# Performance work log

Hardware: AMD Instinct MI355X
Metric: run time of the kernel (lower is better)

Reference implementation:

```python
import jax, jax.numpy as jnp
import numpy as np

N = 50000        # num_nodes
E = 1_600_000    # num_edges (before self loops)
IN = 128         # in_channels
C = 16           # out_channels per head
H = 4            # heads
ED = 16          # edge_dim
SLOPE = 0.2      # LeakyReLU negative slope


def setup_inputs() -> dict:
    key = jax.random.key(0)
    ks = jax.random.split(key, 9)
    x = jax.random.normal(ks[0], (N, IN), jnp.float32)
    edge_index = jax.random.randint(ks[1], (2, E), 0, N)
    edge_attr = jax.random.normal(ks[2], (E, ED), jnp.float32)
    # GATConv parameters (PyG layout): node lin (no bias), attention vectors, edge lin
    W = jax.random.normal(ks[3], (IN, H * C), jnp.float32) / np.float32(np.sqrt(IN))
    att_src = jax.random.normal(ks[4], (H, C), jnp.float32) / np.float32(np.sqrt(C))
    att_dst = jax.random.normal(ks[5], (H, C), jnp.float32) / np.float32(np.sqrt(C))
    W_edge = jax.random.normal(ks[6], (ED, H * C), jnp.float32) / np.float32(np.sqrt(ED))
    att_edge = jax.random.normal(ks[7], (H, C), jnp.float32) / np.float32(np.sqrt(C))
    bias = jnp.zeros((H * C,), jnp.float32)
    return {"x": x, "edge_index": edge_index, "edge_attr": edge_attr,
            "W": W, "att_src": att_src, "att_dst": att_dst,
            "W_edge": W_edge, "att_edge": att_edge, "bias": bias}


def reference(x, edge_index, edge_attr, W, att_src, att_dst, W_edge, att_edge, bias):
    num_nodes = x.shape[0]
    # GATLayer: add self loops (PyG fills self-loop edge_attr with 1.0)
    loops = jnp.arange(num_nodes, dtype=edge_index.dtype)
    ei = jnp.concatenate([edge_index, jnp.stack([loops, loops])], axis=1)
    ea = jnp.concatenate(
        [edge_attr, jnp.ones((num_nodes, edge_attr.shape[1]), edge_attr.dtype)], axis=0)
    src, dst = ei[0], ei[1]  # messages flow src -> dst
    # eval mode: feat_dropout / edge_dropout are no-ops
    h = (x @ W).reshape(num_nodes, H, C)              # [N,H,C]
    a_src = jnp.einsum('nhc,hc->nh', h, att_src)       # [N,H]
    a_dst = jnp.einsum('nhc,hc->nh', h, att_dst)       # [N,H]
    e = (ea @ W_edge).reshape(-1, H, C)                # [E',H,C]
    a_e = jnp.einsum('ehc,hc->eh', e, att_edge)        # [E',H]
    alpha = a_src[src] + a_dst[dst] + a_e              # per-edge logits [E',H]
    alpha = jax.nn.leaky_relu(alpha, SLOPE)
    # segment softmax over incoming edges of each dst node (every node has a self loop)
    amax = jax.ops.segment_max(alpha, dst, num_segments=num_nodes)
    ex = jnp.exp(alpha - amax[dst])
    denom = jax.ops.segment_sum(ex, dst, num_segments=num_nodes)
    att = ex / denom[dst]                              # [E',H]
    # scatter-add aggregation of weighted source features
    out = jax.ops.segment_sum(att[:, :, None] * h[src], dst, num_segments=num_nodes)
    return out.reshape(num_nodes, H * C) + bias        # concat heads + bias
```

## Files before the change

kernel.cpp:

```cpp
#include <hip/hip_runtime.h>
#include <hip/hip_bf16.h>
#include <cstdint>

#define IN_CH 128
#define HC    64
#define ED    16
#define SLOPE 0.2f

__device__ __forceinline__ uint32_t f2bf(float x) {
  uint32_t b = __float_as_uint(x);
  return (b + 0x7fffu + ((b >> 16) & 1u)) >> 16;
}
__device__ __forceinline__ float bf2f(uint32_t h) {
  return __uint_as_float(h << 16);
}

__global__ __launch_bounds__(256) void k_node(
    const float* __restrict__ x, const float* __restrict__ W,
    const float* __restrict__ att_src_p, const float* __restrict__ att_dst_p,
    float* __restrict__ h, float* __restrict__ a_src, float* __restrict__ a_dst,
    int N)
{
  int lane = threadIdx.x & 63;
  int gw = (blockIdx.x * blockDim.x + threadIdx.x) >> 6;
  int nwaves = (gridDim.x * blockDim.x) >> 6;
  float asv = att_src_p[lane];
  float adv = att_dst_p[lane];
  for (int n0 = gw * 4; n0 < N; n0 += nwaves * 4) {
    int n1 = min(n0 + 1, N - 1), n2 = min(n0 + 2, N - 1), n3 = min(n0 + 3, N - 1);
    const float4* xa = (const float4*)(x + (size_t)n0 * IN_CH);
    const float4* xb = (const float4*)(x + (size_t)n1 * IN_CH);
    const float4* xc = (const float4*)(x + (size_t)n2 * IN_CH);
    const float4* xd = (const float4*)(x + (size_t)n3 * IN_CH);
    float acc0 = 0.f, acc1 = 0.f, acc2 = 0.f, acc3 = 0.f;
#pragma unroll 4
    for (int k4 = 0; k4 < IN_CH / 4; k4++) {
      float4 va = xa[k4], vb = xb[k4], vc = xc[k4], vd = xd[k4];
      float w0 = W[(k4 * 4 + 0) * HC + lane];
      float w1 = W[(k4 * 4 + 1) * HC + lane];
      float w2 = W[(k4 * 4 + 2) * HC + lane];
      float w3 = W[(k4 * 4 + 3) * HC + lane];
      acc0 += va.x * w0 + va.y * w1 + va.z * w2 + va.w * w3;
      acc1 += vb.x * w0 + vb.y * w1 + vb.z * w2 + vb.w * w3;
      acc2 += vc.x * w0 + vc.y * w1 + vc.z * w2 + vc.w * w3;
      acc3 += vd.x * w0 + vd.y * w1 + vd.z * w2 + vd.w * w3;
    }
    h[(size_t)n0 * HC + lane] = acc0;
    if (n0 + 1 < N) h[(size_t)n1 * HC + lane] = acc1;
    if (n0 + 2 < N) h[(size_t)n2 * HC + lane] = acc2;
    if (n0 + 3 < N) h[(size_t)n3 * HC + lane] = acc3;
    float s0 = acc0 * asv, s1 = acc1 * asv, s2 = acc2 * asv, s3 = acc3 * asv;
    float d0 = acc0 * adv, d1 = acc1 * adv, d2 = acc2 * adv, d3 = acc3 * adv;
#pragma unroll
    for (int m = 1; m < 16; m <<= 1) {
      s0 += __shfl_xor(s0, m); s1 += __shfl_xor(s1, m);
      s2 += __shfl_xor(s2, m); s3 += __shfl_xor(s3, m);
      d0 += __shfl_xor(d0, m); d1 += __shfl_xor(d1, m);
      d2 += __shfl_xor(d2, m); d3 += __shfl_xor(d3, m);
    }
    if ((lane & 15) == 0) {
      int hh = lane >> 4;
      a_src[(size_t)n0 * 4 + hh] = s0; a_dst[(size_t)n0 * 4 + hh] = d0;
      if (n0 + 1 < N) { a_src[(size_t)n1 * 4 + hh] = s1; a_dst[(size_t)n1 * 4 + hh] = d1; }
      if (n0 + 2 < N) { a_src[(size_t)n2 * 4 + hh] = s2; a_dst[(size_t)n2 * 4 + hh] = d2; }
      if (n0 + 3 < N) { a_src[(size_t)n3 * 4 + hh] = s3; a_dst[(size_t)n3 * 4 + hh] = d3; }
    }
  }
}

__global__ __launch_bounds__(256) void k_hist(const int* __restrict__ dst, int E,
                                              int* __restrict__ deg)
{
  int e = blockIdx.x * 256 + threadIdx.x;
  if (e < E) atomicAdd(&deg[dst[e]], 1);
}

__global__ __launch_bounds__(256) void k_scan_a(const int* __restrict__ deg, int N,
                                                int* __restrict__ rowptr,
                                                int* __restrict__ blksums)
{
  __shared__ int tsum[256];
  int tid = threadIdx.x;
  int base = blockIdx.x * 2048 + tid * 8;
  int pre[8];
  int s = 0;
#pragma unroll
  for (int j = 0; j < 8; j++) {
    int idx = base + j;
    int v = (idx < N) ? deg[idx] : 0;
    pre[j] = s; s += v;
  }
  tsum[tid] = s;
  __syncthreads();
  for (int offm = 1; offm < 256; offm <<= 1) {
    int t = (tid >= offm) ? tsum[tid - offm] : 0;
    __syncthreads();
    tsum[tid] += t;
    __syncthreads();
  }
  int excl = tsum[tid] - s;
#pragma unroll
  for (int j = 0; j < 8; j++) {
    int idx = base + j;
    if (idx < N) rowptr[idx] = excl + pre[j];
  }
  if (tid == 255) blksums[blockIdx.x] = tsum[255];
}

__global__ void k_scan_b(int* __restrict__ blksums, int NB)
{
  if (threadIdx.x == 0 && blockIdx.x == 0) {
    int run = 0;
    for (int b = 0; b < NB; b++) { int t = blksums[b]; blksums[b] = run; run += t; }
  }
}

__global__ __launch_bounds__(256) void k_scan_c(int* __restrict__ rowptr,
                                                const int* __restrict__ blksums,
                                                int N, int E)
{
  int i = blockIdx.x * 256 + threadIdx.x;
  if (i < N) rowptr[i] += blksums[i >> 11];
  if (i == 0) rowptr[N] = E;
}

__global__ __launch_bounds__(256) void k_edge3(
    const int* __restrict__ ei, const float* __restrict__ ea,
    const float* __restrict__ W_edge, const float* __restrict__ att_edge,
    const float* __restrict__ a_src, const float* __restrict__ a_dst,
    const int* __restrict__ rowptr, int* __restrict__ cursor,
    uint4* __restrict__ pay, int E)
{
  __shared__ float ve[ED * 4];
  if (threadIdx.x < 64) {
    int d = threadIdx.x >> 2, hh = threadIdx.x & 3;
    float s = 0.f;
#pragma unroll
    for (int c = 0; c < 16; c++) s += W_edge[d * HC + hh * 16 + c] * att_edge[hh * 16 + c];
    ve[d * 4 + hh] = s;
  }
  __syncthreads();
  int e = blockIdx.x * 256 + threadIdx.x;
  if (e >= E) return;
  int sn = ei[e], dn = ei[E + e];
  float4 as4 = *(const float4*)(a_src + (size_t)sn * 4);
  float4 ad4 = *(const float4*)(a_dst + (size_t)dn * 4);
  const float4* ea4 = (const float4*)(ea + (size_t)e * ED);
  float4 q0 = ea4[0], q1 = ea4[1], q2 = ea4[2], q3 = ea4[3];
  float eav[16] = {q0.x,q0.y,q0.z,q0.w, q1.x,q1.y,q1.z,q1.w,
                   q2.x,q2.y,q2.z,q2.w, q3.x,q3.y,q3.z,q3.w};
  float ae0 = 0.f, ae1 = 0.f, ae2 = 0.f, ae3 = 0.f;
#pragma unroll
  for (int d = 0; d < ED; d++) {
    float v = eav[d];
    ae0 += v * ve[d * 4 + 0]; ae1 += v * ve[d * 4 + 1];
    ae2 += v * ve[d * 4 + 2]; ae3 += v * ve[d * 4 + 3];
  }
  float al0 = as4.x + ad4.x + ae0;
  float al1 = as4.y + ad4.y + ae1;
  float al2 = as4.z + ad4.z + ae2;
  float al3 = as4.w + ad4.w + ae3;
  al0 = al0 > 0.f ? al0 : SLOPE * al0;
  al1 = al1 > 0.f ? al1 : SLOPE * al1;
  al2 = al2 > 0.f ? al2 : SLOPE * al2;
  al3 = al3 > 0.f ? al3 : SLOPE * al3;
  int pos = rowptr[dn] + atomicAdd(&cursor[dn], 1);
  uint4 r;
  r.x = (uint32_t)sn;
  r.y = f2bf(__expf(al0)) | (f2bf(__expf(al1)) << 16);
  r.z = f2bf(__expf(al2)) | (f2bf(__expf(al3)) << 16);
  r.w = 0u;
  pay[pos] = r;
}

__global__ __launch_bounds__(256) void k_agg3(
    const float* __restrict__ h,
    const float* __restrict__ a_src, const float* __restrict__ a_dst,
    const float* __restrict__ W_edge, const float* __restrict__ att_edge,
    const float* __restrict__ bias, const int* __restrict__ rowptr,
    const uint4* __restrict__ pay, float* __restrict__ out, int N)
{
  __shared__ float aes[4];
  if (threadIdx.x < 4) {
    int hh = threadIdx.x;
    float s = 0.f;
    for (int d = 0; d < ED; d++) {
      float vd = 0.f;
#pragma unroll
      for (int c = 0; c < 16; c++) vd += W_edge[d * HC + hh * 16 + c] * att_edge[hh * 16 + c];
      s += vd;
    }
    aes[hh] = s;
  }
  __syncthreads();
  int lane = threadIdx.x & 63;
  int n = blockIdx.x * 4 + (threadIdx.x >> 6);
  if (n >= N) return;
  int hq = lane >> 4;
  int b = rowptr[n], e = rowptr[n + 1];
  float acc = 0.f, den = 0.f;
  int p = b;
  for (; p + 3 < e; p += 4) {
    uint4 r0 = pay[p], r1 = pay[p + 1], r2 = pay[p + 2], r3 = pay[p + 3];
    uint32_t w0 = (hq & 2) ? r0.z : r0.y;
    uint32_t w1 = (hq & 2) ? r1.z : r1.y;
    uint32_t w2 = (hq & 2) ? r2.z : r2.y;
    uint32_t w3 = (hq & 2) ? r3.z : r3.y;
    float e0 = bf2f((hq & 1) ? (w0 >> 16) : (w0 & 0xffffu));
    float e1 = bf2f((hq & 1) ? (w1 >> 16) : (w1 & 0xffffu));
    float e2 = bf2f((hq & 1) ? (w2 >> 16) : (w2 & 0xffffu));
    float e3 = bf2f((hq & 1) ? (w3 >> 16) : (w3 & 0xffffu));
    float h0 = h[(size_t)r0.x * HC + lane];
    float h1 = h[(size_t)r1.x * HC + lane];
    float h2 = h[(size_t)r2.x * HC + lane];
    float h3 = h[(size_t)r3.x * HC + lane];
    acc += e0 * h0 + e1 * h1 + e2 * h2 + e3 * h3;
    den += (e0 + e1) + (e2 + e3);
  }
  for (; p < e; p++) {
    uint4 r0 = pay[p];
    uint32_t w0 = (hq & 2) ? r0.z : r0.y;
    float e0 = bf2f((hq & 1) ? (w0 >> 16) : (w0 & 0xffffu));
    acc += e0 * h[(size_t)r0.x * HC + lane];
    den += e0;
  }
  float al = a_src[(size_t)n * 4 + hq] + a_dst[(size_t)n * 4 + hq] + aes[hq];
  al = al > 0.f ? al : SLOPE * al;
  float exs = __expf(al);
  acc += exs * h[(size_t)n * HC + lane];
  den += exs;
  out[(size_t)n * HC + lane] = acc / den + bias[lane];
}

extern "C" void kernel_launch(void* const* d_in, const int* in_sizes, int n_in,
                              void* d_out, int out_size, void* d_ws, size_t ws_size,
                              hipStream_t stream)
{
  const float* x        = (const float*)d_in[0];
  const int*   ei       = (const int*)d_in[1];
  const float* ea       = (const float*)d_in[2];
  const float* W        = (const float*)d_in[3];
  const float* att_src  = (const float*)d_in[4];
  const float* att_dst  = (const float*)d_in[5];
  const float* W_edge   = (const float*)d_in[6];
  const float* att_edge = (const float*)d_in[7];
  const float* bias     = (const float*)d_in[8];
  float* out = (float*)d_out;

  int N = in_sizes[0] / IN_CH;
  int E = in_sizes[1] / 2;

  uint8_t* ws = (uint8_t*)d_ws;
  size_t off = 0;
  auto alloc = [&](size_t bytes) -> void* {
    void* p = ws + off;
    off = (off + bytes + 255) & ~(size_t)255;
    return p;
  };
  float* h        = (float*)alloc((size_t)N * HC * 4);
  float* a_src_w  = (float*)alloc((size_t)N * 4 * 4);
  float* a_dst_w  = (float*)alloc((size_t)N * 4 * 4);
  int*   deg      = (int*)alloc((size_t)N * 2 * 4);
  int*   cursor   = deg + N;
  int*   rowptr   = (int*)alloc(((size_t)N + 1) * 4);
  int*   blksums  = (int*)alloc(64 * 4);
  uint4* pay      = (uint4*)alloc((size_t)E * 16);
  (void)ws_size; (void)n_in; (void)out_size;

  hipMemsetAsync(deg, 0, (size_t)N * 2 * 4, stream);

  k_node<<<512, 256, 0, stream>>>(x, W, att_src, att_dst, h, a_src_w, a_dst_w, N);
  k_hist<<<(E + 255) / 256, 256, 0, stream>>>(ei + E, E, deg);
  int NB = (N + 2047) / 2048;
  k_scan_a<<<NB, 256, 0, stream>>>(deg, N, rowptr, blksums);
  k_scan_b<<<1, 64, 0, stream>>>(blksums, NB);
  k_scan_c<<<(N + 255) / 256, 256, 0, stream>>>(rowptr, blksums, N, E);
  k_edge3<<<(E + 255) / 256, 256, 0, stream>>>(ei, ea, W_edge, att_edge,
                                               a_src_w, a_dst_w, rowptr, cursor,
                                               pay, E);
  k_agg3<<<(N + 3) / 4, 256, 0, stream>>>(h, a_src_w, a_dst_w, W_edge, att_edge,
                                          bias, rowptr, pay, out, N);
}
```

Measured before the change: 506.2 us.

## Store node features as bf16, add nontemporal loads, precompute scatter cursor offsets

Node features h are now stored as bf16 instead of fp32, which halves the bytes moved by the random gathers in the aggregation kernel. Streaming inputs (x, edge_attr, edge indices, payload) are read with nontemporal loads and the output is written with a nontemporal store, to keep cache space for the gathered data. The scan now initialises the cursor array to rowptr, so the edge kernel skips one rowptr load per edge. The cost is bf16 rounding of h in the aggregation.

```diff
diff --git a/kernel.cpp b/kernel.cpp
--- a/kernel.cpp
+++ b/kernel.cpp
@@ -7,6 +7,9 @@
 #define ED    16
 #define SLOPE 0.2f
 
+typedef float        f32x4 __attribute__((ext_vector_type(4)));
+typedef unsigned int u32x4 __attribute__((ext_vector_type(4)));
+
 __device__ __forceinline__ uint32_t f2bf(float x) {
   uint32_t b = __float_as_uint(x);
   return (b + 0x7fffu + ((b >> 16) & 1u)) >> 16;
@@ -18,7 +21,7 @@
 __global__ __launch_bounds__(256) void k_node(
     const float* __restrict__ x, const float* __restrict__ W,
     const float* __restrict__ att_src_p, const float* __restrict__ att_dst_p,
-    float* __restrict__ h, float* __restrict__ a_src, float* __restrict__ a_dst,
+    uint16_t* __restrict__ hb, float* __restrict__ a_src, float* __restrict__ a_dst,
     int N)
 {
   int lane = threadIdx.x & 63;
@@ -28,14 +31,17 @@
   float adv = att_dst_p[lane];
   for (int n0 = gw * 4; n0 < N; n0 += nwaves * 4) {
     int n1 = min(n0 + 1, N - 1), n2 = min(n0 + 2, N - 1), n3 = min(n0 + 3, N - 1);
-    const float4* xa = (const float4*)(x + (size_t)n0 * IN_CH);
-    const float4* xb = (const float4*)(x + (size_t)n1 * IN_CH);
-    const float4* xc = (const float4*)(x + (size_t)n2 * IN_CH);
-    const float4* xd = (const float4*)(x + (size_t)n3 * IN_CH);
+    const f32x4* xa = (const f32x4*)(x + (size_t)n0 * IN_CH);
+    const f32x4* xb = (const f32x4*)(x + (size_t)n1 * IN_CH);
+    const f32x4* xc = (const f32x4*)(x + (size_t)n2 * IN_CH);
+    const f32x4* xd = (const f32x4*)(x + (size_t)n3 * IN_CH);
     float acc0 = 0.f, acc1 = 0.f, acc2 = 0.f, acc3 = 0.f;
 #pragma unroll 4
     for (int k4 = 0; k4 < IN_CH / 4; k4++) {
-      float4 va = xa[k4], vb = xb[k4], vc = xc[k4], vd = xd[k4];
+      f32x4 va = __builtin_nontemporal_load(xa + k4);
+      f32x4 vb = __builtin_nontemporal_load(xb + k4);
+      f32x4 vc = __builtin_nontemporal_load(xc + k4);
+      f32x4 vd = __builtin_nontemporal_load(xd + k4);
       float w0 = W[(k4 * 4 + 0) * HC + lane];
       float w1 = W[(k4 * 4 + 1) * HC + lane];
       float w2 = W[(k4 * 4 + 2) * HC + lane];
@@ -45,10 +51,10 @@
       acc2 += vc.x * w0 + vc.y * w1 + vc.z * w2 + vc.w * w3;
       acc3 += vd.x * w0 + vd.y * w1 + vd.z * w2 + vd.w * w3;
     }
-    h[(size_t)n0 * HC + lane] = acc0;
-    if (n0 + 1 < N) h[(size_t)n1 * HC + lane] = acc1;
-    if (n0 + 2 < N) h[(size_t)n2 * HC + lane] = acc2;
-    if (n0 + 3 < N) h[(size_t)n3 * HC + lane] = acc3;
+    hb[(size_t)n0 * HC + lane] = (uint16_t)f2bf(acc0);
+    if (n0 + 1 < N) hb[(size_t)n1 * HC + lane] = (uint16_t)f2bf(acc1);
+    if (n0 + 2 < N) hb[(size_t)n2 * HC + lane] = (uint16_t)f2bf(acc2);
+    if (n0 + 3 < N) hb[(size_t)n3 * HC + lane] = (uint16_t)f2bf(acc3);
     float s0 = acc0 * asv, s1 = acc1 * asv, s2 = acc2 * asv, s3 = acc3 * asv;
     float d0 = acc0 * adv, d1 = acc1 * adv, d2 = acc2 * adv, d3 = acc3 * adv;
 #pragma unroll
@@ -72,7 +78,7 @@
                                               int* __restrict__ deg)
 {
   int e = blockIdx.x * 256 + threadIdx.x;
-  if (e < E) atomicAdd(&deg[dst[e]], 1);
+  if (e < E) atomicAdd(&deg[__builtin_nontemporal_load(dst + e)], 1);
 }
 
 __global__ __launch_bounds__(256) void k_scan_a(const int* __restrict__ deg, int N,
@@ -116,20 +122,24 @@
 }
 
 __global__ __launch_bounds__(256) void k_scan_c(int* __restrict__ rowptr,
+                                                int* __restrict__ cursor,
                                                 const int* __restrict__ blksums,
                                                 int N, int E)
 {
   int i = blockIdx.x * 256 + threadIdx.x;
-  if (i < N) rowptr[i] += blksums[i >> 11];
+  if (i < N) {
+    int v = rowptr[i] + blksums[i >> 11];
+    rowptr[i] = v;
+    cursor[i] = v;
+  }
   if (i == 0) rowptr[N] = E;
 }
 
-__global__ __launch_bounds__(256) void k_edge3(
+__global__ __launch_bounds__(256) void k_edge4(
     const int* __restrict__ ei, const float* __restrict__ ea,
     const float* __restrict__ W_edge, const float* __restrict__ att_edge,
     const float* __restrict__ a_src, const float* __restrict__ a_dst,
-    const int* __restrict__ rowptr, int* __restrict__ cursor,
-    uint4* __restrict__ pay, int E)
+    int* __restrict__ cursor, u32x4* __restrict__ pay, int E)
 {
   __shared__ float ve[ED * 4];
   if (threadIdx.x < 64) {
@@ -142,11 +152,15 @@
   __syncthreads();
   int e = blockIdx.x * 256 + threadIdx.x;
   if (e >= E) return;
-  int sn = ei[e], dn = ei[E + e];
+  int sn = __builtin_nontemporal_load(ei + e);
+  int dn = __builtin_nontemporal_load(ei + E + e);
   float4 as4 = *(const float4*)(a_src + (size_t)sn * 4);
   float4 ad4 = *(const float4*)(a_dst + (size_t)dn * 4);
-  const float4* ea4 = (const float4*)(ea + (size_t)e * ED);
-  float4 q0 = ea4[0], q1 = ea4[1], q2 = ea4[2], q3 = ea4[3];
+  const f32x4* ea4 = (const f32x4*)(ea + (size_t)e * ED);
+  f32x4 q0 = __builtin_nontemporal_load(ea4 + 0);
+  f32x4 q1 = __builtin_nontemporal_load(ea4 + 1);
+  f32x4 q2 = __builtin_nontemporal_load(ea4 + 2);
+  f32x4 q3 = __builtin_nontemporal_load(ea4 + 3);
   float eav[16] = {q0.x,q0.y,q0.z,q0.w, q1.x,q1.y,q1.z,q1.w,
                    q2.x,q2.y,q2.z,q2.w, q3.x,q3.y,q3.z,q3.w};
   float ae0 = 0.f, ae1 = 0.f, ae2 = 0.f, ae3 = 0.f;
@@ -164,8 +178,8 @@
   al1 = al1 > 0.f ? al1 : SLOPE * al1;
   al2 = al2 > 0.f ? al2 : SLOPE * al2;
   al3 = al3 > 0.f ? al3 : SLOPE * al3;
-  int pos = rowptr[dn] + atomicAdd(&cursor[dn], 1);
-  uint4 r;
+  int pos = atomicAdd(&cursor[dn], 1);
+  u32x4 r;
   r.x = (uint32_t)sn;
   r.y = f2bf(__expf(al0)) | (f2bf(__expf(al1)) << 16);
   r.z = f2bf(__expf(al2)) | (f2bf(__expf(al3)) << 16);
@@ -173,12 +187,12 @@
   pay[pos] = r;
 }
 
-__global__ __launch_bounds__(256) void k_agg3(
-    const float* __restrict__ h,
+__global__ __launch_bounds__(256) void k_agg4(
+    const uint16_t* __restrict__ hb,
     const float* __restrict__ a_src, const float* __restrict__ a_dst,
     const float* __restrict__ W_edge, const float* __restrict__ att_edge,
     const float* __restrict__ bias, const int* __restrict__ rowptr,
-    const uint4* __restrict__ pay, float* __restrict__ out, int N)
+    const u32x4* __restrict__ pay, float* __restrict__ out, int N)
 {
   __shared__ float aes[4];
   if (threadIdx.x < 4) {
@@ -201,7 +215,10 @@
   float acc = 0.f, den = 0.f;
   int p = b;
   for (; p + 3 < e; p += 4) {
-    uint4 r0 = pay[p], r1 = pay[p + 1], r2 = pay[p + 2], r3 = pay[p + 3];
+    u32x4 r0 = __builtin_nontemporal_load(pay + p);
+    u32x4 r1 = __builtin_nontemporal_load(pay + p + 1);
+    u32x4 r2 = __builtin_nontemporal_load(pay + p + 2);
+    u32x4 r3 = __builtin_nontemporal_load(pay + p + 3);
     uint32_t w0 = (hq & 2) ? r0.z : r0.y;
     uint32_t w1 = (hq & 2) ? r1.z : r1.y;
     uint32_t w2 = (hq & 2) ? r2.z : r2.y;
@@ -210,26 +227,26 @@
     float e1 = bf2f((hq & 1) ? (w1 >> 16) : (w1 & 0xffffu));
     float e2 = bf2f((hq & 1) ? (w2 >> 16) : (w2 & 0xffffu));
     float e3 = bf2f((hq & 1) ? (w3 >> 16) : (w3 & 0xffffu));
-    float h0 = h[(size_t)r0.x * HC + lane];
-    float h1 = h[(size_t)r1.x * HC + lane];
-    float h2 = h[(size_t)r2.x * HC + lane];
-    float h3 = h[(size_t)r3.x * HC + lane];
+    float h0 = bf2f(hb[(size_t)r0.x * HC + lane]);
+    float h1 = bf2f(hb[(size_t)r1.x * HC + lane]);
+    float h2 = bf2f(hb[(size_t)r2.x * HC + lane]);
+    float h3 = bf2f(hb[(size_t)r3.x * HC + lane]);
     acc += e0 * h0 + e1 * h1 + e2 * h2 + e3 * h3;
     den += (e0 + e1) + (e2 + e3);
   }
   for (; p < e; p++) {
-    uint4 r0 = pay[p];
+    u32x4 r0 = __builtin_nontemporal_load(pay + p);
     uint32_t w0 = (hq & 2) ? r0.z : r0.y;
     float e0 = bf2f((hq & 1) ? (w0 >> 16) : (w0 & 0xffffu));
-    acc += e0 * h[(size_t)r0.x * HC + lane];
+    acc += e0 * bf2f(hb[(size_t)r0.x * HC + lane]);
     den += e0;
   }
   float al = a_src[(size_t)n * 4 + hq] + a_dst[(size_t)n * 4 + hq] + aes[hq];
   al = al > 0.f ? al : SLOPE * al;
   float exs = __expf(al);
-  acc += exs * h[(size_t)n * HC + lane];
+  acc += exs * bf2f(hb[(size_t)n * HC + lane]);
   den += exs;
-  out[(size_t)n * HC + lane] = acc / den + bias[lane];
+  __builtin_nontemporal_store(acc / den + bias[lane], out + (size_t)n * HC + lane);
 }
 
 extern "C" void kernel_launch(void* const* d_in, const int* in_sizes, int n_in,
@@ -257,27 +274,26 @@
     off = (off + bytes + 255) & ~(size_t)255;
     return p;
   };
-  float* h        = (float*)alloc((size_t)N * HC * 4);
+  uint16_t* hb    = (uint16_t*)alloc((size_t)N * HC * 2);
   float* a_src_w  = (float*)alloc((size_t)N * 4 * 4);
   float* a_dst_w  = (float*)alloc((size_t)N * 4 * 4);
-  int*   deg      = (int*)alloc((size_t)N * 2 * 4);
-  int*   cursor   = deg + N;
+  int*   deg      = (int*)alloc((size_t)N * 4);
+  int*   cursor   = (int*)alloc((size_t)N * 4);
   int*   rowptr   = (int*)alloc(((size_t)N + 1) * 4);
   int*   blksums  = (int*)alloc(64 * 4);
-  uint4* pay      = (uint4*)alloc((size_t)E * 16);
+  u32x4* pay      = (u32x4*)alloc((size_t)E * 16);
   (void)ws_size; (void)n_in; (void)out_size;
 
-  hipMemsetAsync(deg, 0, (size_t)N * 2 * 4, stream);
-
-  k_node<<<512, 256, 0, stream>>>(x, W, att_src, att_dst, h, a_src_w, a_dst_w, N);
+  hipMemsetAsync(deg, 0, (size_t)N * 4, stream);
+
+  k_node<<<512, 256, 0, stream>>>(x, W, att_src, att_dst, hb, a_src_w, a_dst_w, N);
   k_hist<<<(E + 255) / 256, 256, 0, stream>>>(ei + E, E, deg);
   int NB = (N + 2047) / 2048;
   k_scan_a<<<NB, 256, 0, stream>>>(deg, N, rowptr, blksums);
   k_scan_b<<<1, 64, 0, stream>>>(blksums, NB);
-  k_scan_c<<<(N + 255) / 256, 256, 0, stream>>>(rowptr, blksums, N, E);
-  k_edge3<<<(E + 255) / 256, 256, 0, stream>>>(ei, ea, W_edge, att_edge,
-                                               a_src_w, a_dst_w, rowptr, cursor,
-                                               pay, E);
-  k_agg3<<<(N + 3) / 4, 256, 0, stream>>>(h, a_src_w, a_dst_w, W_edge, att_edge,
+  k_scan_c<<<(N + 255) / 256, 256, 0, stream>>>(rowptr, cursor, blksums, N, E);
+  k_edge4<<<(E + 255) / 256, 256, 0, stream>>>(ei, ea, W_edge, att_edge,
+                                               a_src_w, a_dst_w, cursor, pay, E);
+  k_agg4<<<(N + 3) / 4, 256, 0, stream>>>(hb, a_src_w, a_dst_w, W_edge, att_edge,
                                           bias, rowptr, pay, out, N);
 }
```

Measured after the change: 526.1 us. 3.9% more time.
